# Kernel optimization log

Hardware: AMD Instinct MI355X
Metric: run time of the kernel (lower is better)

The kernel has to match this reference:

```python
import jax, jax.numpy as jnp
import numpy as np

EMB = 256   # EMB_SIZE hard-coded in source
H = 8       # num heads (all heads share the same Q/K/V, as in source)
DK = EMB // H  # 32
B, T = 16, 2048
LN_EPS = 1e-5


def _layernorm(a, g, b):
    m = jnp.mean(a, axis=-1, keepdims=True)
    v = jnp.mean(jnp.square(a - m), axis=-1, keepdims=True)
    return (a - m) * jax.lax.rsqrt(v + LN_EPS) * g + b


def setup_inputs() -> dict:
    key = jax.random.key(0)
    ks = jax.random.split(key, 8)
    sc = 0.02
    return {
        "x": jax.random.normal(ks[0], (B, T, EMB), jnp.float32),
        "Wq": jax.random.normal(ks[1], (EMB, DK), jnp.float32) * sc,
        "Wk": jax.random.normal(ks[2], (EMB, DK), jnp.float32) * sc,
        "Wv": jax.random.normal(ks[3], (EMB, DK), jnp.float32) * sc,
        "Wp": jax.random.normal(ks[4], (EMB, EMB), jnp.float32) * sc,
        "bp": jnp.zeros((EMB,), jnp.float32),
        "W1": jax.random.normal(ks[5], (EMB, 4 * EMB), jnp.float32) * sc,
        "b1": jnp.zeros((4 * EMB,), jnp.float32),
        "W2": jax.random.normal(ks[6], (4 * EMB, EMB), jnp.float32) * sc,
        "b2": jnp.zeros((EMB,), jnp.float32),
        "g1": jnp.ones((EMB,), jnp.float32),
        "be1": jnp.zeros((EMB,), jnp.float32),
        "g2": jnp.ones((EMB,), jnp.float32),
        "be2": jnp.zeros((EMB,), jnp.float32),
    }


def reference(x, Wq, Wk, Wv, Wp, bp, W1, b1, W2, b2, g1, be1, g2, be2):
    # Single shared-head QKV projections (bias-free), as in source
    q = x @ Wq  # [B,T,DK]
    k = x @ Wk
    v = x @ Wv
    # Causal self-attention with explicit score matrix [B,T,T]
    scores = jnp.einsum("btd,bsd->bts", q, k) / jnp.sqrt(jnp.float32(DK))
    causal = jnp.tril(jnp.ones((T, T), dtype=bool))
    scores = jnp.where(causal, scores, -jnp.inf)
    a = jax.nn.softmax(scores, axis=-1)
    attn = jnp.einsum("bts,bsd->btd", a, v)  # [B,T,DK]
    # Source concatenates h identical copies of the same attention output
    cat = jnp.tile(attn, (1, 1, H))  # [B,T,EMB]
    mh = cat @ Wp + bp
    y1 = _layernorm(x + mh, g1, be1)
    ff = jax.nn.gelu(y1 @ W1 + b1, approximate=False) @ W2 + b2
    return _layernorm(y1 + ff, g2, be2)
```

## Files before the change

kernel.cpp:

```cpp
#include <hip/hip_runtime.h>

#define BB 16
#define TT 2048
#define EE 256
#define DK 32
#define MM (BB*TT)
#define FF 1024

typedef __bf16 bf16_t;
typedef __bf16 bf16x8 __attribute__((ext_vector_type(8)));
typedef __bf16 bf16x4 __attribute__((ext_vector_type(4)));
typedef float  f32x4  __attribute__((ext_vector_type(4)));

__device__ __forceinline__ f32x4 mfma16(bf16x8 a, bf16x8 b, f32x4 c){
  return __builtin_amdgcn_mfma_f32_16x16x32_bf16(a, b, c, 0, 0, 0);
}
__device__ __forceinline__ void gload_lds16(const void* g, void* l){
  __builtin_amdgcn_global_load_lds((__attribute__((address_space(1))) void*)g,
                                   (__attribute__((address_space(3))) void*)l,
                                   16, 0, 0);
}

__launch_bounds__(256)
__global__ void prep_kernel(const float* __restrict__ Wq, const float* __restrict__ Wk,
                            const float* __restrict__ Wv, const float* __restrict__ Wp,
                            const float* __restrict__ W1, const float* __restrict__ W2,
                            bf16_t* __restrict__ wqkv, float* __restrict__ wpe,
                            bf16_t* __restrict__ w1t, bf16_t* __restrict__ w2t)
{
  const int i = blockIdx.x*256 + threadIdx.x;
  if (i < 96*256) {
    const int r = i >> 8, c = i & 255;
    float v;
    if (r < 32)      v = Wq[c*32 + r] * 0.17677669529663687f;
    else if (r < 64) v = Wk[c*32 + (r-32)];
    else             v = Wv[c*32 + (r-64)];
    wqkv[i] = (bf16_t)v;
  }
  if (i < 32*256) {
    const int d = i >> 8, n = i & 255;
    float s = 0.f;
    #pragma unroll
    for (int h = 0; h < 8; ++h) s += Wp[(h*32 + d)*256 + n];
    wpe[i] = s;
  }
  if (i < 1024*256) {
    const int n = i >> 8, k = i & 255;
    w1t[i] = (bf16_t)W1[(size_t)k*1024 + n];
  }
  if (i < 256*1024) {
    const int n = i >> 10, k = i & 1023;
    w2t[i] = (bf16_t)W2[(size_t)k*256 + n];
  }
}

__launch_bounds__(256)
__global__ void qkv_kernel(const float* __restrict__ x, const bf16_t* __restrict__ wqkv,
                           bf16_t* __restrict__ q, bf16_t* __restrict__ kd,
                           bf16_t* __restrict__ vT)
{
  __shared__ bf16_t Ws[96*256];
  bf16_t* Vt = Ws;
  const int tid = threadIdx.x;
  #pragma unroll
  for (int i = 0; i < 12; ++i) {
    const int v8  = tid + i*256;
    const int row = v8 >> 5;
    const int bir = (v8 & 31) * 16;
    *(bf16x8*)((char*)Ws + row*512 + (bir ^ ((row & 7) << 4))) =
        *(const bf16x8*)(wqkv + (size_t)v8*8);
  }
  __syncthreads();

  const int w = tid >> 6, l = tid & 63;
  const int lr = l & 15, lk4 = l >> 4, lkb = lk4*8;
  const int m0 = blockIdx.x * 64;
  const int arow = m0 + w*16 + lr;
  const float* xr = x + (size_t)arow * 256;

  f32x4 acc[6] = {};
  #pragma unroll
  for (int s = 0; s < 8; ++s) {
    const int kb = s*32 + lkb;
    const float4 v0 = *(const float4*)(xr + kb);
    const float4 v1 = *(const float4*)(xr + kb + 4);
    bf16x8 a;
    a[0]=(bf16_t)v0.x; a[1]=(bf16_t)v0.y; a[2]=(bf16_t)v0.z; a[3]=(bf16_t)v0.w;
    a[4]=(bf16_t)v1.x; a[5]=(bf16_t)v1.y; a[6]=(bf16_t)v1.z; a[7]=(bf16_t)v1.w;
    #pragma unroll
    for (int j = 0; j < 6; ++j) {
      const int nrow = j*16 + lr;
      const bf16x8 bf = *(const bf16x8*)((const char*)Ws + nrow*512 +
                                         ((kb*2) ^ ((nrow & 7) << 4)));
      acc[j] = mfma16(a, bf, acc[j]);
    }
  }
  #pragma unroll
  for (int j = 0; j < 4; ++j) {
    #pragma unroll
    for (int r = 0; r < 4; ++r) {
      const int orow = m0 + w*16 + lk4*4 + r;
      const int col  = j*16 + lr;
      const bf16_t v = (bf16_t)acc[j][r];
      if (col < 32) q[(size_t)orow*32 + col] = v;
      else          kd[(size_t)orow*32 + (col-32)] = v;
    }
  }
  __syncthreads();
  #pragma unroll
  for (int j = 4; j < 6; ++j)
    #pragma unroll
    for (int r = 0; r < 4; ++r) {
      const int d = (j-4)*16 + lr;
      const int t = w*16 + lk4*4 + r;
      *(bf16_t*)((char*)Vt + d*128 + ((((t>>3) ^ (d&7))<<4) | ((t&7)*2))) =
          (bf16_t)acc[j][r];
    }
  __syncthreads();
  {
    const int d = tid >> 3, c8 = tid & 7;
    const bf16x8 v = *(const bf16x8*)((char*)Vt + d*128 + ((c8 ^ (d&7))<<4));
    *(bf16x8*)(vT + ((size_t)(m0 >> 11)*32 + d)*TT + (m0 & 2047) + c8*8) = v;
  }
}

__launch_bounds__(256)
__global__ void attnp_kernel(const bf16_t* __restrict__ q, const bf16_t* __restrict__ kd,
                             const bf16_t* __restrict__ vT,
                             float* __restrict__ part_acc, float* __restrict__ part_ml)
{
  __shared__ bf16_t P[4][16*128];
  const int tid = threadIdx.x;
  const int w = tid >> 6, l = tid & 63;
  const int wv = blockIdx.x*4 + w;
  const int lr = l & 15, g4 = l >> 4;
  const float NEG_INF = -__builtin_inff();

  const int b = wv / 320;
  const int u = wv - b*320;
  int r, base;
  if      (u >= 192) { r = 3; base = 192; }
  else if (u >= 96)  { r = 2; base = 96;  }
  else if (u >= 32)  { r = 1; base = 32;  }
  else               { r = 0; base = 0;   }
  const int qq = u - base;
  const int g  = r*32 + qq / (r+1);
  const int c  = qq - (qq / (r+1))*(r+1);
  const int t_total = (g >> 3) + 1;
  const int t0 = c*4;
  const int t1 = min(t0 + 4, t_total);

  const bf16_t* qb = q  + (size_t)b*TT*32;
  const bf16_t* kb = kd + (size_t)b*TT*32;
  const bf16_t* vb = vT + (size_t)b*32*TT;
  const int q0 = g*16;
  const int qg = q0 + lr;

  const bf16x8 qa = *(const bf16x8*)(qb + (size_t)(q0 + lr)*32 + g4*8);
  const bf16_t* v0r = vb + (size_t)lr*TT;
  const bf16_t* v1r = vb + (size_t)(16 + lr)*TT;

  f32x4 acc0 = {0.f,0.f,0.f,0.f}, acc1 = {0.f,0.f,0.f,0.f};
  float mrun = NEG_INF, lsum = 0.f;
  char* pb = (char*)&P[w][0];
  const int swz = (lr & 7) << 4;
  const f32x4 zf = {0.f,0.f,0.f,0.f};

  for (int t = t0; t < t1; ++t) {
    const int k0 = t * 128;
    f32x4 s[8];
    #pragma unroll
    for (int cc = 0; cc < 8; ++cc) {
      const bf16x8 kf = *(const bf16x8*)(kb + (size_t)(k0 + cc*16 + lr)*32 + g4*8);
      s[cc] = mfma16(kf, qa, zf);
    }
    if (t == t_total - 1) {
      #pragma unroll
      for (int cc = 0; cc < 8; ++cc)
        #pragma unroll
        for (int rr = 0; rr < 4; ++rr)
          if (k0 + cc*16 + g4*4 + rr > qg) s[cc][rr] = NEG_INF;
    }
    float mt = NEG_INF;
    #pragma unroll
    for (int cc = 0; cc < 8; ++cc) {
      float a01 = fmaxf(s[cc][0], s[cc][1]), a23 = fmaxf(s[cc][2], s[cc][3]);
      mt = fmaxf(mt, fmaxf(a01, a23));
    }
    mt = fmaxf(mt, __shfl_xor(mt, 16));
    mt = fmaxf(mt, __shfl_xor(mt, 32));
    const float mn = fmaxf(mrun, mt);
    const float sc = __expf(mrun - mn);
    float ps = 0.f;
    #pragma unroll
    for (int cc = 0; cc < 8; ++cc) {
      float p0 = __expf(s[cc][0]-mn), p1 = __expf(s[cc][1]-mn);
      float p2 = __expf(s[cc][2]-mn), p3 = __expf(s[cc][3]-mn);
      s[cc][0]=p0; s[cc][1]=p1; s[cc][2]=p2; s[cc][3]=p3;
      ps += (p0+p1) + (p2+p3);
    }
    ps += __shfl_xor(ps, 16);
    ps += __shfl_xor(ps, 32);
    lsum = lsum*sc + ps;
    mrun = mn;
    acc0 *= sc; acc1 *= sc;
    #pragma unroll
    for (int cc = 0; cc < 8; ++cc) {
      bf16x4 pk;
      pk[0]=(bf16_t)s[cc][0]; pk[1]=(bf16_t)s[cc][1];
      pk[2]=(bf16_t)s[cc][2]; pk[3]=(bf16_t)s[cc][3];
      *(bf16x4*)(pb + lr*256 + ((cc*32 + g4*8) ^ swz)) = pk;
    }
    #pragma unroll
    for (int h = 0; h < 4; ++h) {
      const bf16x8 pbf = *(const bf16x8*)(pb + lr*256 + ((h*64 + g4*16) ^ swz));
      acc0 = mfma16(*(const bf16x8*)(v0r + k0 + h*32 + g4*8), pbf, acc0);
      acc1 = mfma16(*(const bf16x8*)(v1r + k0 + h*32 + g4*8), pbf, acc1);
    }
  }
  float* pa = part_acc + (size_t)wv*512;
  *(f32x4*)(pa + l*8)     = acc0;
  *(f32x4*)(pa + l*8 + 4) = acc1;
  if (l < 16) {
    part_ml[wv*32 + l]      = mrun;
    part_ml[wv*32 + 16 + l] = lsum;
  }
}

__launch_bounds__(256)
__global__ void attnc_kernel(const float* __restrict__ part_acc,
                             const float* __restrict__ part_ml,
                             bf16_t* __restrict__ attn)
{
  const int tid = threadIdx.x;
  const int id = blockIdx.x*4 + (tid >> 6);
  const int l = tid & 63, lr = l & 15, g4 = l >> 4;
  const int b = id >> 7, g = id & 127;
  const int r = g >> 5;
  const int base = (r == 0) ? 0 : (r == 1) ? 32 : (r == 2) ? 96 : 192;
  const int p0 = b*320 + base + (g - (r << 5))*(r + 1);
  const int nc = r + 1;
  const float NEG_INF = -__builtin_inff();

  float m0v=NEG_INF,m1v=NEG_INF,m2v=NEG_INF,m3v=NEG_INF;
  float l0v=0,l1v=0,l2v=0,l3v=0;
  f32x4 a00={0,0,0,0},a01={0,0,0,0},a10={0,0,0,0},a11={0,0,0,0};
  f32x4 a20={0,0,0,0},a21={0,0,0,0},a30={0,0,0,0},a31={0,0,0,0};
  {
    const float* pa = part_acc + (size_t)p0*512;
    a00 = *(const f32x4*)(pa + l*8); a01 = *(const f32x4*)(pa + l*8 + 4);
    m0v = part_ml[p0*32 + lr]; l0v = part_ml[p0*32 + 16 + lr];
  }
  if (nc > 1) {
    const float* pa = part_acc + (size_t)(p0+1)*512;
    a10 = *(const f32x4*)(pa + l*8); a11 = *(const f32x4*)(pa + l*8 + 4);
    m1v = part_ml[(p0+1)*32 + lr]; l1v = part_ml[(p0+1)*32 + 16 + lr];
  }
  if (nc > 2) {
    const float* pa = part_acc + (size_t)(p0+2)*512;
    a20 = *(const f32x4*)(pa + l*8); a21 = *(const f32x4*)(pa + l*8 + 4);
    m2v = part_ml[(p0+2)*32 + lr]; l2v = part_ml[(p0+2)*32 + 16 + lr];
  }
  if (nc > 3) {
    const float* pa = part_acc + (size_t)(p0+3)*512;
    a30 = *(const f32x4*)(pa + l*8); a31 = *(const f32x4*)(pa + l*8 + 4);
    m3v = part_ml[(p0+3)*32 + lr]; l3v = part_ml[(p0+3)*32 + 16 + lr];
  }
  const float M = fmaxf(fmaxf(m0v, m1v), fmaxf(m2v, m3v));
  const float w0 = __expf(m0v - M), w1 = __expf(m1v - M);
  const float w2 = __expf(m2v - M), w3 = __expf(m3v - M);
  const float L = l0v*w0 + l1v*w1 + l2v*w2 + l3v*w3;
  const float inv = 1.0f / L;
  f32x4 o0 = (a00*w0 + a10*w1 + a20*w2 + a30*w3) * inv;
  f32x4 o1 = (a01*w0 + a11*w1 + a21*w2 + a31*w3) * inv;

  bf16_t* ao = attn + ((size_t)b*TT + g*16 + lr)*32;
  bf16x4 ob0, ob1;
  ob0[0]=(bf16_t)o0[0]; ob0[1]=(bf16_t)o0[1]; ob0[2]=(bf16_t)o0[2]; ob0[3]=(bf16_t)o0[3];
  ob1[0]=(bf16_t)o1[0]; ob1[1]=(bf16_t)o1[1]; ob1[2]=(bf16_t)o1[2]; ob1[3]=(bf16_t)o1[3];
  *(bf16x4*)(ao + g4*4)      = ob0;
  *(bf16x4*)(ao + 16 + g4*4) = ob1;
}

__launch_bounds__(256)
__global__ void ln1_kernel(const float* __restrict__ x, const bf16_t* __restrict__ attn,
                           const float* __restrict__ wpe, const float* __restrict__ bp,
                           const float* __restrict__ g1, const float* __restrict__ be1,
                           bf16_t* __restrict__ y1b)
{
  __shared__ float Wp_s[32*256];
  const int tid = threadIdx.x;
  for (int i = tid; i < 32*64; i += 256)
    ((float4*)Wp_s)[i] = ((const float4*)wpe)[i];
  __syncthreads();

  const int w = tid >> 6, l = tid & 63;
  const int n = l * 4;
  const float4 gv  = *(const float4*)(g1  + n);
  const float4 bev = *(const float4*)(be1 + n);
  const float4 bpv = *(const float4*)(bp  + n);

  #pragma unroll 1
  for (int it = 0; it < 8; ++it) {
    const int row = blockIdx.x*32 + it*4 + w;
    const bf16_t* ar = attn + (size_t)row*32;
    float a[32];
    #pragma unroll
    for (int i = 0; i < 4; ++i) {
      const bf16x8 t = *(const bf16x8*)(ar + i*8);
      #pragma unroll
      for (int j = 0; j < 8; ++j) a[i*8 + j] = (float)t[j];
    }
    float mh[4] = {bpv.x, bpv.y, bpv.z, bpv.w};
    #pragma unroll
    for (int d = 0; d < 32; ++d) {
      const float4 wv = *(const float4*)(Wp_s + d*256 + n);
      const float ad = a[d];
      mh[0] = fmaf(ad, wv.x, mh[0]); mh[1] = fmaf(ad, wv.y, mh[1]);
      mh[2] = fmaf(ad, wv.z, mh[2]); mh[3] = fmaf(ad, wv.w, mh[3]);
    }
    const float4 xv = *(const float4*)(x + (size_t)row*256 + n);
    const float t0 = xv.x + mh[0], t1 = xv.y + mh[1];
    const float t2 = xv.z + mh[2], t3 = xv.w + mh[3];
    float s1 = (t0+t1) + (t2+t3);
    float s2 = (t0*t0 + t1*t1) + (t2*t2 + t3*t3);
    #pragma unroll
    for (int m = 1; m < 64; m <<= 1) { s1 += __shfl_xor(s1, m); s2 += __shfl_xor(s2, m); }
    const float mean = s1 * (1.0f/256.0f);
    const float var  = s2 * (1.0f/256.0f) - mean*mean;
    const float rs   = rsqrtf(var + 1e-5f);
    float4 yv;
    yv.x = (t0-mean)*rs*gv.x + bev.x; yv.y = (t1-mean)*rs*gv.y + bev.y;
    yv.z = (t2-mean)*rs*gv.z + bev.z; yv.w = (t3-mean)*rs*gv.w + bev.w;
    bf16x4 yb; yb[0]=(bf16_t)yv.x; yb[1]=(bf16_t)yv.y; yb[2]=(bf16_t)yv.z; yb[3]=(bf16_t)yv.w;
    *(bf16x4*)(y1b + (size_t)row*256 + n) = yb;
  }
}

__launch_bounds__(1024)
__global__ void mlp_kernel(const bf16_t* __restrict__ y1b, const bf16_t* __restrict__ w1t,
                           const float* __restrict__ b1, const bf16_t* __restrict__ w2t,
                           const float* __restrict__ b2, const float* __restrict__ g2,
                           const float* __restrict__ be2, float* __restrict__ out)
{
  __shared__ char SM[151552];
  const int tid = threadIdx.x;
  const int w = tid >> 6, l = tid & 63;
  const int lr = l & 15, g4 = l >> 4;
  const int m0 = blockIdx.x * 128;
  const int wm  = (w >> 1) * 16;
  const int wn1 = (w & 1) * 32;
  const int wn2 = (w & 1) * 128;

  *(float*)(SM + 147456 + tid*4) = b1[tid];
  asm volatile("s_waitcnt vmcnt(0) lgkmcnt(0)" ::: "memory");
  __builtin_amdgcn_sched_barrier(0);

  #define ST_W1(i, d)                                                         \
    { _Pragma("unroll")                                                       \
      for (int p_ = 0; p_ < 2; ++p_) {                                        \
        const int idx_ = p_*1024 + tid;                                       \
        const int r_ = idx_ >> 5, c_ = idx_ & 31;                             \
        const int sc_ = (c_ & 24) | ((c_ ^ r_) & 7);                          \
        gload_lds16(w1t + (size_t)((i)*64 + r_)*256 + sc_*8,                  \
                    SM + (d)*32768 + idx_*16);                                \
      } }
  #define ST_W2(i, d)                                                         \
    { _Pragma("unroll")                                                       \
      for (int p_ = 0; p_ < 2; ++p_) {                                        \
        const int idx_ = p_*1024 + tid;                                       \
        const int r_ = idx_ >> 3, c_ = idx_ & 7;                              \
        gload_lds16(w2t + (size_t)r_*1024 + (i)*64 + ((c_ ^ r_) & 7)*8,       \
                    SM + 65536 + (d)*32768 + idx_*16);                        \
      } }

  ST_W1(0, 0);
  bf16x8 aA[8];
  #pragma unroll
  for (int kk = 0; kk < 8; ++kk)
    aA[kk] = *(const bf16x8*)(y1b + (size_t)(m0 + wm + lr)*256 + kk*32 + g4*8);
  ST_W2(0, 0);
  ST_W1(1, 1);

  f32x4 oacc[8] = {};
  char* hb = SM + 131072;

  #pragma unroll 1
  for (int i = 0; i < 16; ++i) {
    if (i < 15) { asm volatile("s_waitcnt vmcnt(4)" ::: "memory"); }
    else        { asm volatile("s_waitcnt vmcnt(2)" ::: "memory"); }
    __builtin_amdgcn_sched_barrier(0);
    __builtin_amdgcn_s_barrier();
    const char* sw1 = SM + (i & 1)*32768;
    f32x4 ah0 = {0.f,0.f,0.f,0.f}, ah1 = {0.f,0.f,0.f,0.f};
    __builtin_amdgcn_s_setprio(1);
    #pragma unroll
    for (int kk = 0; kk < 8; ++kk) {
      const int off = kk*64 + g4*16;
      const int n0r = wn1 + lr, n1r = wn1 + 16 + lr;
      const bf16x8 bf0 = *(const bf16x8*)(sw1 + n0r*512 + (off ^ ((n0r & 7) << 4)));
      const bf16x8 bf1 = *(const bf16x8*)(sw1 + n1r*512 + (off ^ ((n1r & 7) << 4)));
      ah0 = mfma16(aA[kk], bf0, ah0);
      ah1 = mfma16(aA[kk], bf1, ah1);
    }
    __builtin_amdgcn_s_setprio(0);
    #pragma unroll
    for (int j = 0; j < 2; ++j) {
      const float bias = *(const float*)(SM + 147456 + (i*64 + wn1 + j*16 + lr)*4);
      const f32x4 av = j ? ah1 : ah0;
      const int hcol2 = (wn1 + j*16 + lr)*2;
      #pragma unroll
      for (int r = 0; r < 4; ++r) {
        const int hrow = wm + g4*4 + r;
        const float v = av[r] + bias;
        const float z = 1.5957691216057308f * v * fmaf(0.044715f, v*v, 1.0f);
        const float gg = v * __builtin_amdgcn_rcpf(1.0f + __expf(-z));
        *(bf16_t*)(hb + hrow*128 + (hcol2 ^ ((hrow & 7) << 4))) = (bf16_t)gg;
      }
    }
    asm volatile("s_waitcnt lgkmcnt(0)" ::: "memory");
    __builtin_amdgcn_sched_barrier(0);
    if (i < 15) { asm volatile("s_waitcnt vmcnt(2)" ::: "memory"); }
    else        { asm volatile("s_waitcnt vmcnt(0)" ::: "memory"); }
    __builtin_amdgcn_sched_barrier(0);
    __builtin_amdgcn_s_barrier();
    const char* sw2 = SM + 65536 + (i & 1)*32768;
    __builtin_amdgcn_s_setprio(1);
    #pragma unroll
    for (int kk2 = 0; kk2 < 2; ++kk2) {
      const int off = kk2*64 + g4*16;
      const int hr = wm + lr;
      const bf16x8 ha = *(const bf16x8*)(hb + hr*128 + (off ^ ((hr & 7) << 4)));
      #pragma unroll
      for (int j3 = 0; j3 < 8; ++j3) {
        const int n = wn2 + j3*16 + lr;
        const bf16x8 wb = *(const bf16x8*)(sw2 + n*128 + (off ^ ((n & 7) << 4)));
        oacc[j3] = mfma16(ha, wb, oacc[j3]);
      }
    }
    __builtin_amdgcn_s_setprio(0);
    if (i < 15) ST_W2(i+1, (i+1)&1);
    if (i < 14) ST_W1(i+2, i&1);
  }
  #undef ST_W1
  #undef ST_W2

  float b2r[8], g2r[8], be2r[8];
  #pragma unroll
  for (int j3 = 0; j3 < 8; ++j3) {
    const int col = wn2 + j3*16 + lr;
    b2r[j3] = b2[col]; g2r[j3] = g2[col]; be2r[j3] = be2[col];
  }
  #pragma unroll
  for (int r = 0; r < 4; ++r) {
    const int grow = m0 + wm + g4*4 + r;
    #pragma unroll
    for (int j3 = 0; j3 < 8; ++j3) {
      const int col = wn2 + j3*16 + lr;
      oacc[j3][r] += b2r[j3] + (float)y1b[(size_t)grow*256 + col];
    }
  }
  __syncthreads();
  float* red = (float*)SM;
  #pragma unroll
  for (int r = 0; r < 4; ++r) {
    float s1 = 0.f, s2 = 0.f;
    #pragma unroll
    for (int j3 = 0; j3 < 8; ++j3) { s1 += oacc[j3][r]; s2 += oacc[j3][r]*oacc[j3][r]; }
    #pragma unroll
    for (int m = 1; m < 16; m <<= 1) { s1 += __shfl_xor(s1, m); s2 += __shfl_xor(s2, m); }
    if (lr == 0) {
      const int rl = wm + g4*4 + r;
      red[rl*4 + (w & 1)*2]     = s1;
      red[rl*4 + (w & 1)*2 + 1] = s2;
    }
  }
  __syncthreads();
  #pragma unroll
  for (int r = 0; r < 4; ++r) {
    const int rl = wm + g4*4 + r;
    const float S1 = red[rl*4+0] + red[rl*4+2];
    const float S2 = red[rl*4+1] + red[rl*4+3];
    const float mean = S1 * (1.0f/256.0f);
    const float var  = S2 * (1.0f/256.0f) - mean*mean;
    const float rs   = rsqrtf(var + 1e-5f);
    #pragma unroll
    for (int j3 = 0; j3 < 8; ++j3) {
      const int col = wn2 + j3*16 + lr;
      out[(size_t)(m0 + rl)*256 + col] = (oacc[j3][r] - mean)*rs*g2r[j3] + be2r[j3];
    }
  }
}

extern "C" void kernel_launch(void* const* d_in, const int* in_sizes, int n_in,
                              void* d_out, int out_size, void* d_ws, size_t ws_size,
                              hipStream_t stream)
{
  const float* x   = (const float*)d_in[0];
  const float* Wq  = (const float*)d_in[1];
  const float* Wk  = (const float*)d_in[2];
  const float* Wv  = (const float*)d_in[3];
  const float* Wp  = (const float*)d_in[4];
  const float* bp  = (const float*)d_in[5];
  const float* W1  = (const float*)d_in[6];
  const float* b1  = (const float*)d_in[7];
  const float* W2  = (const float*)d_in[8];
  const float* b2  = (const float*)d_in[9];
  const float* g1  = (const float*)d_in[10];
  const float* be1 = (const float*)d_in[11];
  const float* g2  = (const float*)d_in[12];
  const float* be2 = (const float*)d_in[13];

  char* ws = (char*)d_ws;
  bf16_t* qd   = (bf16_t*)(ws + ((size_t)0  << 20));
  bf16_t* kd   = (bf16_t*)(ws + ((size_t)2  << 20));
  bf16_t* vTd  = (bf16_t*)(ws + ((size_t)4  << 20));
  bf16_t* attn = (bf16_t*)(ws + ((size_t)6  << 20));
  bf16_t* y1b  = (bf16_t*)(ws + ((size_t)8  << 20));
  bf16_t* wqkv = (bf16_t*)(ws + ((size_t)24 << 20));
  float*  wpe  = (float*) (ws + ((size_t)25 << 20));
  bf16_t* w1t  = (bf16_t*)(ws + ((size_t)26 << 20));
  bf16_t* w2t  = (bf16_t*)(ws + ((size_t)27 << 20));
  float*  pml  = (float*) (ws + ((size_t)28 << 20));
  float*  pacc = (float*) (ws + ((size_t)29 << 20));
  float* out = (float*)d_out;

  prep_kernel<<<1024, 256, 0, stream>>>(Wq, Wk, Wv, Wp, W1, W2, wqkv, wpe, w1t, w2t);
  qkv_kernel<<<512, 256, 0, stream>>>(x, wqkv, qd, kd, vTd);
  attnp_kernel<<<1280, 256, 0, stream>>>(qd, kd, vTd, pacc, pml);
  attnc_kernel<<<512, 256, 0, stream>>>(pacc, pml, attn);
  ln1_kernel<<<1024, 256, 0, stream>>>(x, attn, wpe, bp, g1, be1, y1b);
  mlp_kernel<<<256, 1024, 0, stream>>>(y1b, w1t, b1, w2t, b2, g2, be2, out);
}
```

Measured before the change: 132.9 us.

## Fuse attention partial-combine with projection and LayerNorm1 using MFMA

Merges the attention split-combine kernel and the LN1 kernel into one kernel. The combined attention tile is kept in swizzled LDS rather than written to global memory. The head-summed Wp is now stored as transposed bf16 so the projection runs on 16x16x32 bf16 MFMA instead of scalar FMAs. This removes one launch and the attn intermediate round-trip, at the cost of more LDS per block, strided per-lane x loads, and bf16 rounding of the projection weights.

```diff
diff --git a/kernel.cpp b/kernel.cpp
--- a/kernel.cpp
+++ b/kernel.cpp
@@ -25,7 +25,7 @@
 __global__ void prep_kernel(const float* __restrict__ Wq, const float* __restrict__ Wk,
                             const float* __restrict__ Wv, const float* __restrict__ Wp,
                             const float* __restrict__ W1, const float* __restrict__ W2,
-                            bf16_t* __restrict__ wqkv, float* __restrict__ wpe,
+                            bf16_t* __restrict__ wqkv, bf16_t* __restrict__ wpT,
                             bf16_t* __restrict__ w1t, bf16_t* __restrict__ w2t)
 {
   const int i = blockIdx.x*256 + threadIdx.x;
@@ -37,12 +37,12 @@
     else             v = Wv[c*32 + (r-64)];
     wqkv[i] = (bf16_t)v;
   }
-  if (i < 32*256) {
-    const int d = i >> 8, n = i & 255;
+  if (i < 256*32) {
+    const int n = i >> 5, k = i & 31;
     float s = 0.f;
     #pragma unroll
-    for (int h = 0; h < 8; ++h) s += Wp[(h*32 + d)*256 + n];
-    wpe[i] = s;
+    for (int h = 0; h < 8; ++h) s += Wp[(h*32 + k)*256 + n];
+    wpT[i] = (bf16_t)s;
   }
   if (i < 1024*256) {
     const int n = i >> 8, k = i & 255;
@@ -228,112 +228,134 @@
 }
 
 __launch_bounds__(256)
-__global__ void attnc_kernel(const float* __restrict__ part_acc,
-                             const float* __restrict__ part_ml,
-                             bf16_t* __restrict__ attn)
+__global__ void ln1f_kernel(const float* __restrict__ part_acc,
+                            const float* __restrict__ part_ml,
+                            const bf16_t* __restrict__ wpT,
+                            const float* __restrict__ bp, const float* __restrict__ x,
+                            const float* __restrict__ g1, const float* __restrict__ be1,
+                            bf16_t* __restrict__ y1b)
 {
+  __shared__ char SM[57344];
+  char* wp_s  = SM;
+  char* att_s = SM + 16384;
+  float* bp_s = (float*)(SM + 20480);
+  char* y_s   = SM + 24576;
   const int tid = threadIdx.x;
-  const int id = blockIdx.x*4 + (tid >> 6);
-  const int l = tid & 63, lr = l & 15, g4 = l >> 4;
+  const int w = tid >> 6, l = tid & 63;
+  const int lr = l & 15, g4 = l >> 4;
+  const float NEG_INF = -__builtin_inff();
+
+  #pragma unroll
+  for (int p = 0; p < 4; ++p) {
+    const int idx = p*256 + tid;
+    const int n = idx >> 2, c = idx & 3;
+    gload_lds16(wpT + (size_t)n*32 + ((c ^ (n & 3)) * 8), wp_s + idx*16);
+  }
+  if (tid < 64) ((float4*)bp_s)[tid] = ((const float4*)bp)[tid];
+
+  const int id = blockIdx.x*4 + w;
   const int b = id >> 7, g = id & 127;
-  const int r = g >> 5;
-  const int base = (r == 0) ? 0 : (r == 1) ? 32 : (r == 2) ? 96 : 192;
-  const int p0 = b*320 + base + (g - (r << 5))*(r + 1);
-  const int nc = r + 1;
-  const float NEG_INF = -__builtin_inff();
-
-  float m0v=NEG_INF,m1v=NEG_INF,m2v=NEG_INF,m3v=NEG_INF;
-  float l0v=0,l1v=0,l2v=0,l3v=0;
-  f32x4 a00={0,0,0,0},a01={0,0,0,0},a10={0,0,0,0},a11={0,0,0,0};
-  f32x4 a20={0,0,0,0},a21={0,0,0,0},a30={0,0,0,0},a31={0,0,0,0};
   {
-    const float* pa = part_acc + (size_t)p0*512;
-    a00 = *(const f32x4*)(pa + l*8); a01 = *(const f32x4*)(pa + l*8 + 4);
-    m0v = part_ml[p0*32 + lr]; l0v = part_ml[p0*32 + 16 + lr];
-  }
-  if (nc > 1) {
-    const float* pa = part_acc + (size_t)(p0+1)*512;
-    a10 = *(const f32x4*)(pa + l*8); a11 = *(const f32x4*)(pa + l*8 + 4);
-    m1v = part_ml[(p0+1)*32 + lr]; l1v = part_ml[(p0+1)*32 + 16 + lr];
-  }
-  if (nc > 2) {
-    const float* pa = part_acc + (size_t)(p0+2)*512;
-    a20 = *(const f32x4*)(pa + l*8); a21 = *(const f32x4*)(pa + l*8 + 4);
-    m2v = part_ml[(p0+2)*32 + lr]; l2v = part_ml[(p0+2)*32 + 16 + lr];
-  }
-  if (nc > 3) {
-    const float* pa = part_acc + (size_t)(p0+3)*512;
-    a30 = *(const f32x4*)(pa + l*8); a31 = *(const f32x4*)(pa + l*8 + 4);
-    m3v = part_ml[(p0+3)*32 + lr]; l3v = part_ml[(p0+3)*32 + 16 + lr];
-  }
-  const float M = fmaxf(fmaxf(m0v, m1v), fmaxf(m2v, m3v));
-  const float w0 = __expf(m0v - M), w1 = __expf(m1v - M);
-  const float w2 = __expf(m2v - M), w3 = __expf(m3v - M);
-  const float L = l0v*w0 + l1v*w1 + l2v*w2 + l3v*w3;
-  const float inv = 1.0f / L;
-  f32x4 o0 = (a00*w0 + a10*w1 + a20*w2 + a30*w3) * inv;
-  f32x4 o1 = (a01*w0 + a11*w1 + a21*w2 + a31*w3) * inv;
-
-  bf16_t* ao = attn + ((size_t)b*TT + g*16 + lr)*32;
-  bf16x4 ob0, ob1;
-  ob0[0]=(bf16_t)o0[0]; ob0[1]=(bf16_t)o0[1]; ob0[2]=(bf16_t)o0[2]; ob0[3]=(bf16_t)o0[3];
-  ob1[0]=(bf16_t)o1[0]; ob1[1]=(bf16_t)o1[1]; ob1[2]=(bf16_t)o1[2]; ob1[3]=(bf16_t)o1[3];
-  *(bf16x4*)(ao + g4*4)      = ob0;
-  *(bf16x4*)(ao + 16 + g4*4) = ob1;
-}
-
-__launch_bounds__(256)
-__global__ void ln1_kernel(const float* __restrict__ x, const bf16_t* __restrict__ attn,
-                           const float* __restrict__ wpe, const float* __restrict__ bp,
-                           const float* __restrict__ g1, const float* __restrict__ be1,
-                           bf16_t* __restrict__ y1b)
-{
-  __shared__ float Wp_s[32*256];
-  const int tid = threadIdx.x;
-  for (int i = tid; i < 32*64; i += 256)
-    ((float4*)Wp_s)[i] = ((const float4*)wpe)[i];
-  __syncthreads();
-
-  const int w = tid >> 6, l = tid & 63;
-  const int n = l * 4;
-  const float4 gv  = *(const float4*)(g1  + n);
-  const float4 bev = *(const float4*)(be1 + n);
-  const float4 bpv = *(const float4*)(bp  + n);
-
-  #pragma unroll 1
-  for (int it = 0; it < 8; ++it) {
-    const int row = blockIdx.x*32 + it*4 + w;
-    const bf16_t* ar = attn + (size_t)row*32;
-    float a[32];
-    #pragma unroll
-    for (int i = 0; i < 4; ++i) {
-      const bf16x8 t = *(const bf16x8*)(ar + i*8);
-      #pragma unroll
-      for (int j = 0; j < 8; ++j) a[i*8 + j] = (float)t[j];
-    }
-    float mh[4] = {bpv.x, bpv.y, bpv.z, bpv.w};
-    #pragma unroll
-    for (int d = 0; d < 32; ++d) {
-      const float4 wv = *(const float4*)(Wp_s + d*256 + n);
-      const float ad = a[d];
-      mh[0] = fmaf(ad, wv.x, mh[0]); mh[1] = fmaf(ad, wv.y, mh[1]);
-      mh[2] = fmaf(ad, wv.z, mh[2]); mh[3] = fmaf(ad, wv.w, mh[3]);
-    }
-    const float4 xv = *(const float4*)(x + (size_t)row*256 + n);
-    const float t0 = xv.x + mh[0], t1 = xv.y + mh[1];
-    const float t2 = xv.z + mh[2], t3 = xv.w + mh[3];
-    float s1 = (t0+t1) + (t2+t3);
-    float s2 = (t0*t0 + t1*t1) + (t2*t2 + t3*t3);
-    #pragma unroll
-    for (int m = 1; m < 64; m <<= 1) { s1 += __shfl_xor(s1, m); s2 += __shfl_xor(s2, m); }
-    const float mean = s1 * (1.0f/256.0f);
-    const float var  = s2 * (1.0f/256.0f) - mean*mean;
+    const int rr = g >> 5;
+    const int base = (rr == 0) ? 0 : (rr == 1) ? 32 : (rr == 2) ? 96 : 192;
+    const int p0 = b*320 + base + (g - (rr << 5))*(rr + 1);
+    const int nc = rr + 1;
+    float M = NEG_INF;
+    float mv0=NEG_INF, mv1=NEG_INF, mv2=NEG_INF, mv3=NEG_INF;
+    float lv0=0, lv1=0, lv2=0, lv3=0;
+    f32x4 a00={0,0,0,0}, a01={0,0,0,0}, a10={0,0,0,0}, a11={0,0,0,0};
+    f32x4 a20={0,0,0,0}, a21={0,0,0,0}, a30={0,0,0,0}, a31={0,0,0,0};
+    {
+      const float* pa = part_acc + (size_t)p0*512;
+      a00 = *(const f32x4*)(pa + l*8); a01 = *(const f32x4*)(pa + l*8 + 4);
+      mv0 = part_ml[p0*32 + lr]; lv0 = part_ml[p0*32 + 16 + lr];
+    }
+    if (nc > 1) {
+      const float* pa = part_acc + (size_t)(p0+1)*512;
+      a10 = *(const f32x4*)(pa + l*8); a11 = *(const f32x4*)(pa + l*8 + 4);
+      mv1 = part_ml[(p0+1)*32 + lr]; lv1 = part_ml[(p0+1)*32 + 16 + lr];
+    }
+    if (nc > 2) {
+      const float* pa = part_acc + (size_t)(p0+2)*512;
+      a20 = *(const f32x4*)(pa + l*8); a21 = *(const f32x4*)(pa + l*8 + 4);
+      mv2 = part_ml[(p0+2)*32 + lr]; lv2 = part_ml[(p0+2)*32 + 16 + lr];
+    }
+    if (nc > 3) {
+      const float* pa = part_acc + (size_t)(p0+3)*512;
+      a30 = *(const f32x4*)(pa + l*8); a31 = *(const f32x4*)(pa + l*8 + 4);
+      mv3 = part_ml[(p0+3)*32 + lr]; lv3 = part_ml[(p0+3)*32 + 16 + lr];
+    }
+    M = fmaxf(fmaxf(mv0, mv1), fmaxf(mv2, mv3));
+    const float w0 = __expf(mv0 - M), w1 = __expf(mv1 - M);
+    const float w2 = __expf(mv2 - M), w3 = __expf(mv3 - M);
+    const float L = lv0*w0 + lv1*w1 + lv2*w2 + lv3*w3;
+    const float inv = 1.0f / L;
+    const f32x4 o0 = (a00*w0 + a10*w1 + a20*w2 + a30*w3) * inv;
+    const f32x4 o1 = (a01*w0 + a11*w1 + a21*w2 + a31*w3) * inv;
+    char* ab = att_s + w*1024;
+    bf16x4 h0, h1;
+    #pragma unroll
+    for (int r = 0; r < 4; ++r) { h0[r] = (bf16_t)o0[r]; h1[r] = (bf16_t)o1[r]; }
+    *(bf16x4*)(ab + lr*64 + ((g4*8)      ^ ((lr & 3) << 4))) = h0;
+    *(bf16x4*)(ab + lr*64 + ((32 + g4*8) ^ ((lr & 3) << 4))) = h1;
+  }
+  __syncthreads();
+
+  const char* ab = att_s + w*1024;
+  const bf16x8 af = *(const bf16x8*)(ab + lr*64 + ((g4*16) ^ ((lr & 3) << 4)));
+  f32x4 acc[16];
+  #pragma unroll
+  for (int j = 0; j < 16; ++j) {
+    const int n = j*16 + lr;
+    const bf16x8 bf = *(const bf16x8*)(wp_s + n*64 + ((g4*16) ^ ((n & 3) << 4)));
+    acc[j] = mfma16(af, bf, f32x4{0,0,0,0});
+  }
+
+  const int row0 = b*TT + g*16;
+  float bb[16];
+  #pragma unroll
+  for (int j = 0; j < 16; ++j) bb[j] = bp_s[j*16 + lr];
+  float s1[4] = {0,0,0,0}, s2[4] = {0,0,0,0};
+  #pragma unroll
+  for (int j = 0; j < 16; ++j)
+    #pragma unroll
+    for (int r = 0; r < 4; ++r) {
+      const float t = acc[j][r] + bb[j] +
+                      x[(size_t)(row0 + g4*4 + r)*256 + j*16 + lr];
+      acc[j][r] = t;
+      s1[r] += t; s2[r] += t*t;
+    }
+  #pragma unroll
+  for (int r = 0; r < 4; ++r) {
+    #pragma unroll
+    for (int m = 1; m < 16; m <<= 1) {
+      s1[r] += __shfl_xor(s1[r], m); s2[r] += __shfl_xor(s2[r], m);
+    }
+  }
+  char* yb = y_s + w*8192;
+  #pragma unroll
+  for (int r = 0; r < 4; ++r) {
+    const float mean = s1[r] * (1.0f/256.0f);
+    const float var  = s2[r] * (1.0f/256.0f) - mean*mean;
     const float rs   = rsqrtf(var + 1e-5f);
-    float4 yv;
-    yv.x = (t0-mean)*rs*gv.x + bev.x; yv.y = (t1-mean)*rs*gv.y + bev.y;
-    yv.z = (t2-mean)*rs*gv.z + bev.z; yv.w = (t3-mean)*rs*gv.w + bev.w;
-    bf16x4 yb; yb[0]=(bf16_t)yv.x; yb[1]=(bf16_t)yv.y; yb[2]=(bf16_t)yv.z; yb[3]=(bf16_t)yv.w;
-    *(bf16x4*)(y1b + (size_t)row*256 + n) = yb;
+    const int mrow = g4*4 + r;
+    #pragma unroll
+    for (int j = 0; j < 16; ++j) {
+      const int col = j*16 + lr;
+      const float yv = (acc[j][r] - mean)*rs*g1[col] + be1[col];
+      *(bf16_t*)(yb + mrow*512 + ((col*2) ^ ((mrow & 7) << 4))) = (bf16_t)yv;
+    }
+  }
+  __syncthreads();
+  {
+    char* ybw = y_s + w*8192;
+    #pragma unroll
+    for (int p = 0; p < 8; ++p) {
+      const int u = p*64 + l;
+      const int mrow = u >> 5, c16 = u & 31;
+      const bf16x8 v = *(const bf16x8*)(ybw + mrow*512 + ((c16*16) ^ ((mrow & 7) << 4)));
+      *(bf16x8*)(y1b + (size_t)(row0 + mrow)*256 + c16*8) = v;
+    }
   }
 }
 
@@ -515,20 +537,18 @@
   bf16_t* qd   = (bf16_t*)(ws + ((size_t)0  << 20));
   bf16_t* kd   = (bf16_t*)(ws + ((size_t)2  << 20));
   bf16_t* vTd  = (bf16_t*)(ws + ((size_t)4  << 20));
-  bf16_t* attn = (bf16_t*)(ws + ((size_t)6  << 20));
   bf16_t* y1b  = (bf16_t*)(ws + ((size_t)8  << 20));
   bf16_t* wqkv = (bf16_t*)(ws + ((size_t)24 << 20));
-  float*  wpe  = (float*) (ws + ((size_t)25 << 20));
+  bf16_t* wpT  = (bf16_t*)(ws + ((size_t)25 << 20));
   bf16_t* w1t  = (bf16_t*)(ws + ((size_t)26 << 20));
   bf16_t* w2t  = (bf16_t*)(ws + ((size_t)27 << 20));
   float*  pml  = (float*) (ws + ((size_t)28 << 20));
   float*  pacc = (float*) (ws + ((size_t)29 << 20));
   float* out = (float*)d_out;
 
-  prep_kernel<<<1024, 256, 0, stream>>>(Wq, Wk, Wv, Wp, W1, W2, wqkv, wpe, w1t, w2t);
+  prep_kernel<<<1024, 256, 0, stream>>>(Wq, Wk, Wv, Wp, W1, W2, wqkv, wpT, w1t, w2t);
   qkv_kernel<<<512, 256, 0, stream>>>(x, wqkv, qd, kd, vTd);
   attnp_kernel<<<1280, 256, 0, stream>>>(qd, kd, vTd, pacc, pml);
-  attnc_kernel<<<512, 256, 0, stream>>>(pacc, pml, attn);
-  ln1_kernel<<<1024, 256, 0, stream>>>(x, attn, wpe, bp, g1, be1, y1b);
+  ln1f_kernel<<<512, 256, 0, stream>>>(pacc, pml, wpT, bp, x, g1, be1, y1b);
   mlp_kernel<<<256, 1024, 0, stream>>>(y1b, w1t, b1, w2t, b2, g2, be2, out);
 }
```

After: 123.2 us. -7.3%, faster.
